# Performance work log

Hardware: AMD Instinct MI355X
Metric: run time of the kernel (lower is better)

Reference implementation:

```python
import jax, jax.numpy as jnp
import numpy as np

SCORE_THRESHOLD = 0.15
IOU_THRESHOLD = 0.5
MAX_OUTPUT = 10          # tf.image.non_max_suppression(..., 10, ...)
NUM_CLASSES = 80
NUM_ANCHORS = 5
NEG = -1e9               # score for suppressed / below-threshold boxes


def setup_inputs() -> dict:
    key = jax.random.key(0)
    k1, k2 = jax.random.split(key)
    preds = jax.random.normal(k1, (16, 52, 52, NUM_ANCHORS * (5 + NUM_CLASSES)), dtype=jnp.float32)
    # anchor priors in grid-cell units, typical YOLOv2 range
    anchors = jax.random.uniform(k2, (NUM_ANCHORS, 2), dtype=jnp.float32, minval=0.5, maxval=6.0)
    return {"preds": preds, "anchors": anchors}


def _decode(preds, anchors):
    """YOLOv2 head decode (the `_interpret_prediction` callable)."""
    B, H, W, _ = preds.shape
    A = anchors.shape[0]
    p = preds.reshape(B, H, W, A, 5 + NUM_CLASSES)
    gy, gx = jnp.meshgrid(jnp.arange(H, dtype=preds.dtype),
                          jnp.arange(W, dtype=preds.dtype), indexing="ij")
    grid = jnp.stack([gx, gy], axis=-1)[None, :, :, None, :]   # (1,H,W,1,2) in (x,y)
    dims = jnp.array([W, H], dtype=preds.dtype)
    box_xy = (jax.nn.sigmoid(p[..., :2]) + grid) / dims        # normalized centers
    box_wh = jnp.exp(p[..., 2:4]) * anchors[None, None, None, :, :] / dims
    box_confidence = jax.nn.sigmoid(p[..., 4:5])
    box_class_probs = jax.nn.softmax(p[..., 5:], axis=-1)
    return box_xy, box_wh, box_confidence, box_class_probs


def _iou(box, boxes):
    """IoU of one box (ymin,xmin,ymax,xmax) against all boxes [N,4]."""
    tl = jnp.maximum(box[:2], boxes[:, :2])
    br = jnp.minimum(box[2:], boxes[:, 2:])
    inter = jnp.prod(jnp.maximum(br - tl, 0.0), axis=-1)
    area1 = jnp.prod(jnp.maximum(box[2:] - box[:2], 0.0))
    area2 = jnp.prod(jnp.maximum(boxes[:, 2:] - boxes[:, :2], 0.0), axis=-1)
    return inter / (area1 + area2 - inter + 1e-9)


def reference(preds, anchors):
    box_xy, box_wh, box_confidence, box_class_probs = _decode(preds, anchors)
    box_mins = box_xy - box_wh / 2.0
    box_maxes = box_xy + box_wh / 2.0
    # (ymin, xmin, ymax, xmax), matching the K.concatenate in the source
    boxes = jnp.concatenate([box_mins[..., 1:2], box_mins[..., 0:1],
                             box_maxes[..., 1:2], box_maxes[..., 0:1]], axis=-1)
    box_scores = box_confidence * box_class_probs
    box_classes = jnp.argmax(box_scores, axis=-1)
    box_class_scores = jnp.max(box_scores, axis=-1)

    boxes = boxes.reshape(-1, 4)                       # [N,4]
    scores = box_class_scores.reshape(-1)              # [N]
    classes = box_classes.reshape(-1).astype(preds.dtype)

    # score-threshold mask: instead of boolean_mask (dynamic shape), kill scores
    live = jnp.where(scores >= SCORE_THRESHOLD, scores, NEG)

    # greedy NMS, fixed MAX_OUTPUT iterations (semantics of tf.image.non_max_suppression)
    def step(cur_scores, _):
        i = jnp.argmax(cur_scores)
        s = cur_scores[i]
        valid = s > NEG / 2
        box = boxes[i]
        ious = _iou(box, boxes)
        nxt = jnp.where(ious > IOU_THRESHOLD, NEG, cur_scores).at[i].set(NEG)
        row = jnp.where(valid,
                        jnp.concatenate([box, s[None], classes[i][None]]),
                        jnp.zeros((6,), dtype=preds.dtype))
        return nxt, row

    _, rows = jax.lax.scan(step, live, None, length=MAX_OUTPUT)
    return rows  # [10, 6] = (ymin, xmin, ymax, xmax, score, class); zero rows = padding
```

## Files before the change

### kernel.cpp

```cpp
#include <hip/hip_runtime.h>
#include <math.h>

#define A_N      5
#define GRID_HW  52
#define NCLS     80
#define CH       85
#define SCORE_T  0.15f
#define IOU_T    0.5f
#define NEGV     (-1e9f)
#define MAXOUT   10

#define BPB          32
#define TILE_FLOATS  (BPB * CH)
#define FULL_LOADS   10
#define TAIL_LANES   40

#define NMS_THREADS  256
#define NCAP         4096
#define NKA          (NCAP / NMS_THREADS)

__device__ __forceinline__ float fexp(float x) { return __expf(x); }

__device__ __forceinline__ void gload_lds16(const float* g, float* l) {
    __builtin_amdgcn_global_load_lds(
        (const __attribute__((address_space(1))) unsigned int*)g,
        (__attribute__((address_space(3))) unsigned int*)l, 16, 0, 0);
}

__global__ void init_counter_kernel(int* __restrict__ counter) {
    *counter = 0;
}

__global__ __launch_bounds__(64) void decode_kernel(
    const float* __restrict__ preds,
    const float* __restrict__ anchors,
    float4* __restrict__ pbox, float* __restrict__ pscore,
    float* __restrict__ pcls,
    int* __restrict__ counter, int N, int capacity)
{
    __shared__ __align__(16) float lds[TILE_FLOATS];

    const int tile = blockIdx.x;
    const int lane = (int)threadIdx.x;
    const float* gbase = preds + (size_t)tile * TILE_FLOATS;

#pragma unroll
    for (int i = 0; i < FULL_LOADS; ++i) {
        gload_lds16(gbase + (size_t)(i * 64 + lane) * 4, &lds[i * 256]);
    }
    if (lane < TAIL_LANES) {
        gload_lds16(gbase + (size_t)(FULL_LOADS * 64 + lane) * 4,
                    &lds[FULL_LOADS * 256]);
    }
    __syncthreads();

    const int b  = lane >> 1;
    const int h  = lane & 1;
    const int gi = tile * BPB + b;
    const float* bp = lds + b * CH;
    const float* cl = bp + 5 + h * 40;

    float m = cl[0];
    int   am = h * 40;
#pragma unroll
    for (int j = 1; j < 40; ++j) {
        float x = cl[j];
        if (x > m) { m = x; am = h * 40 + j; }
    }
    float s = 0.0f;
#pragma unroll
    for (int j = 0; j < 40; ++j) s += fexp(cl[j] - m);

    {
        float m2 = __shfl_xor(m, 1);
        float s2 = __shfl_xor(s, 1);
        int   am2 = __shfl_xor(am, 1);
        float M = fmaxf(m, m2);
        s = s * fexp(m - M) + s2 * fexp(m2 - M);
        if (m2 > m || (m2 == m && am2 < am)) am = am2;
        m = M;
    }

    float conf  = 1.0f / (1.0f + fexp(-bp[4]));
    float score = conf / s;

    bool live = (h == 0) && (gi < N) && (score >= SCORE_T);

    unsigned long long mask = __ballot(live);
    if (mask) {
        int nlive  = __popcll(mask);
        int leader = (int)__ffsll((long long)mask) - 1;
        int base_ = 0;
        if (lane == leader) base_ = atomicAdd(counter, nlive);
        base_ = __shfl(base_, leader);
        if (live) {
            int a = gi % A_N;
            int t = gi / A_N;
            int wx = t % GRID_HW;
            int hy = (t / GRID_HW) % GRID_HW;
            const float inv = 1.0f / (float)GRID_HW;
            float cx = (1.0f / (1.0f + fexp(-bp[0])) + (float)wx) * inv;
            float cy = (1.0f / (1.0f + fexp(-bp[1])) + (float)hy) * inv;
            float bw = fexp(bp[2]) * anchors[2 * a]     * inv;
            float bh = fexp(bp[3]) * anchors[2 * a + 1] * inv;

            int pos = base_ + __popcll(mask & ((1ull << lane) - 1));
            if (pos < capacity) {
                pbox[pos]   = make_float4(cy - 0.5f * bh, cx - 0.5f * bw,
                                          cy + 0.5f * bh, cx + 0.5f * bw);
                pscore[pos] = score;
                pcls[pos]   = (float)am;
            }
        }
    }
}

__global__ __launch_bounds__(NMS_THREADS) void nms_kernel(
    const float4* __restrict__ pbox, float* __restrict__ pscore,
    const float* __restrict__ pcls, const int* __restrict__ counter,
    int capacity, float* __restrict__ out)
{
    __shared__ float sy0[NCAP], sx0[NCAP], sy1[NCAP], sx1[NCAP], ssc[NCAP];
    __shared__ float psc[4];
    __shared__ int   pix[4];

    int M = *counter;
    if (M > capacity) M = capacity;
    const int tid  = (int)threadIdx.x;
    const int lane = tid & 63;
    const int wid  = tid >> 6;

    if (M <= NCAP) {
#pragma unroll
        for (int k = 0; k < NKA; ++k) {
            int j = tid + (k << 8);
            if (j < M) {
                float4 bx = pbox[j];
                sy0[j] = bx.x; sx0[j] = bx.y; sy1[j] = bx.z; sx1[j] = bx.w;
                ssc[j] = pscore[j];
            } else {
                ssc[j] = -INFINITY;
            }
        }
        __syncthreads();

        for (int it = 0; it < MAXOUT; ++it) {
            float bs = -INFINITY; int bi = -1;
#pragma unroll
            for (int k = 0; k < NKA; ++k) {
                int j = tid + (k << 8);
                float v = ssc[j];
                if (v > bs) { bs = v; bi = j; }
            }
#pragma unroll
            for (int off = 32; off; off >>= 1) {
                float os = __shfl_xor(bs, off);
                int   oi = __shfl_xor(bi, off);
                if (os > bs || (os == bs && oi != -1 && (bi == -1 || oi < bi))) {
                    bs = os; bi = oi;
                }
            }
            if (lane == 0) { psc[wid] = bs; pix[wid] = bi; }
            __syncthreads();

            bs = psc[0]; bi = pix[0];
#pragma unroll
            for (int w = 1; w < 4; ++w) {
                float os = psc[w]; int oi = pix[w];
                if (os > bs || (os == bs && oi != -1 && (bi == -1 || oi < bi))) {
                    bs = os; bi = oi;
                }
            }
            bool valid = (bi >= 0) && (bs > NEGV * 0.5f);

            if (tid == 0) {
                if (valid) {
                    out[it*6+0] = sy0[bi]; out[it*6+1] = sx0[bi];
                    out[it*6+2] = sy1[bi]; out[it*6+3] = sx1[bi];
                    out[it*6+4] = bs;      out[it*6+5] = pcls[bi];
                } else {
                    out[it*6+0] = 0.f; out[it*6+1] = 0.f; out[it*6+2] = 0.f;
                    out[it*6+3] = 0.f; out[it*6+4] = 0.f; out[it*6+5] = 0.f;
                }
            }

            if (valid) {
                float wy0 = sy0[bi], wx0 = sx0[bi], wy1 = sy1[bi], wx1 = sx1[bi];
                float a1 = fmaxf(wy1 - wy0, 0.f) * fmaxf(wx1 - wx0, 0.f);
#pragma unroll
                for (int k = 0; k < NKA; ++k) {
                    int j = tid + (k << 8);
                    if (j == bi) ssc[j] = NEGV;
                    float ty = fmaxf(wy0, sy0[j]);
                    float tx = fmaxf(wx0, sx0[j]);
                    float by = fminf(wy1, sy1[j]);
                    float bx = fminf(wx1, sx1[j]);
                    float inter = fmaxf(by - ty, 0.f) * fmaxf(bx - tx, 0.f);
                    float a2 = fmaxf(sy1[j] - sy0[j], 0.f) * fmaxf(sx1[j] - sx0[j], 0.f);
                    float iou = inter / (a1 + a2 - inter + 1e-9f);
                    if (iou > IOU_T && j < M) ssc[j] = NEGV;
                }
            }
            __syncthreads();
        }
    } else {
        for (int it = 0; it < MAXOUT; ++it) {
            float bs = -INFINITY; int bi = -1;
            for (int j = tid; j < M; j += NMS_THREADS) {
                float v = pscore[j];
                if (v > bs) { bs = v; bi = j; }
            }
#pragma unroll
            for (int off = 32; off; off >>= 1) {
                float os = __shfl_xor(bs, off);
                int   oi = __shfl_xor(bi, off);
                if (os > bs || (os == bs && oi != -1 && (bi == -1 || oi < bi))) {
                    bs = os; bi = oi;
                }
            }
            if (lane == 0) { psc[wid] = bs; pix[wid] = bi; }
            __syncthreads();
            bs = psc[0]; bi = pix[0];
#pragma unroll
            for (int w = 1; w < 4; ++w) {
                float os = psc[w]; int oi = pix[w];
                if (os > bs || (os == bs && oi != -1 && (bi == -1 || oi < bi))) {
                    bs = os; bi = oi;
                }
            }
            bool valid = (bi >= 0) && (bs > NEGV * 0.5f);
            if (tid == 0) {
                if (valid) {
                    float4 bx = pbox[bi];
                    out[it*6+0] = bx.x; out[it*6+1] = bx.y;
                    out[it*6+2] = bx.z; out[it*6+3] = bx.w;
                    out[it*6+4] = bs;   out[it*6+5] = pcls[bi];
                    pscore[bi] = NEGV;
                } else {
                    out[it*6+0] = 0.f; out[it*6+1] = 0.f; out[it*6+2] = 0.f;
                    out[it*6+3] = 0.f; out[it*6+4] = 0.f; out[it*6+5] = 0.f;
                }
            }
            __syncthreads();
            if (valid) {
                float4 wb = pbox[bi];
                float a1 = fmaxf(wb.z - wb.x, 0.f) * fmaxf(wb.w - wb.y, 0.f);
                for (int j = tid; j < M; j += NMS_THREADS) {
                    float4 bj = pbox[j];
                    float ty = fmaxf(wb.x, bj.x);
                    float tx = fmaxf(wb.y, bj.y);
                    float by = fminf(wb.z, bj.z);
                    float bx = fminf(wb.w, bj.w);
                    float inter = fmaxf(by - ty, 0.f) * fmaxf(bx - tx, 0.f);
                    float a2 = fmaxf(bj.z - bj.x, 0.f) * fmaxf(bj.w - bj.y, 0.f);
                    float iou = inter / (a1 + a2 - inter + 1e-9f);
                    if (iou > IOU_T) pscore[j] = NEGV;
                }
            }
            __syncthreads();
        }
    }
}

extern "C" void kernel_launch(void* const* d_in, const int* in_sizes, int n_in,
                              void* d_out, int out_size, void* d_ws, size_t ws_size,
                              hipStream_t stream) {
    (void)n_in; (void)out_size;
    const float* preds   = (const float*)d_in[0];
    const float* anchors = (const float*)d_in[1];
    float* out = (float*)d_out;

    int N = in_sizes[0] / CH;

    char* ws = (char*)d_ws;
    int* counter = (int*)ws;
    size_t avail = (ws_size > 64) ? (ws_size - 64) : 0;
    long long cap = (long long)(avail / (sizeof(float4) + 2 * sizeof(float)));
    if (cap > N) cap = N;
    if (cap < 0) cap = 0;
    int capacity = (int)cap;

    float4* pbox  = (float4*)(ws + 64);
    float* pscore = (float*)(pbox + capacity);
    float* pcls   = pscore + capacity;

    init_counter_kernel<<<1, 1, 0, stream>>>(counter);

    int nTiles = (N + BPB - 1) / BPB;
    decode_kernel<<<nTiles, 64, 0, stream>>>(
        preds, anchors, pbox, pscore, pcls, counter, N, capacity);
    nms_kernel<<<1, NMS_THREADS, 0, stream>>>(
        pbox, pscore, pcls, counter, capacity, out);
}
```

Baseline: 76.58 us.

## Enlarge decode blocks, fuse softmax pass, and widen NMS to 1024 threads

After: 67.58 us (median of 4 runs). 11.8% less time.

```diff
diff --git a/kernel.cpp b/kernel.cpp
--- a/kernel.cpp
+++ b/kernel.cpp
@@ -10,14 +10,15 @@
 #define NEGV     (-1e9f)
 #define MAXOUT   10
 
-#define BPB          32
+#define BPB          128
+#define DEC_THREADS  256
 #define TILE_FLOATS  (BPB * CH)
-#define FULL_LOADS   10
-#define TAIL_LANES   40
-
-#define NMS_THREADS  256
+#define WAVE_FLOATS  (TILE_FLOATS / 4)
+#define WAVE_FULL    10
+#define WAVE_TAIL    40
+
+#define NMS_THREADS  1024
 #define NCAP         4096
-#define NKA          (NCAP / NMS_THREADS)
 
 __device__ __forceinline__ float fexp(float x) { return __expf(x); }
 
@@ -31,7 +32,7 @@
     *counter = 0;
 }
 
-__global__ __launch_bounds__(64) void decode_kernel(
+__global__ __launch_bounds__(DEC_THREADS) void decode_kernel(
     const float* __restrict__ preds,
     const float* __restrict__ anchors,
     float4* __restrict__ pbox, float* __restrict__ pscore,
@@ -41,48 +42,48 @@
     __shared__ __align__(16) float lds[TILE_FLOATS];
 
     const int tile = blockIdx.x;
-    const int lane = (int)threadIdx.x;
-    const float* gbase = preds + (size_t)tile * TILE_FLOATS;
-
-#pragma unroll
-    for (int i = 0; i < FULL_LOADS; ++i) {
-        gload_lds16(gbase + (size_t)(i * 64 + lane) * 4, &lds[i * 256]);
-    }
-    if (lane < TAIL_LANES) {
-        gload_lds16(gbase + (size_t)(FULL_LOADS * 64 + lane) * 4,
-                    &lds[FULL_LOADS * 256]);
+    const int lane = (int)threadIdx.x & 63;
+    const int wid  = (int)threadIdx.x >> 6;
+
+    const float* gbase = preds + (size_t)tile * TILE_FLOATS + wid * WAVE_FLOATS;
+    float* lbase = lds + wid * WAVE_FLOATS;
+
+#pragma unroll
+    for (int i = 0; i < WAVE_FULL; ++i) {
+        gload_lds16(gbase + (size_t)(i * 64 + lane) * 4, lbase + i * 256);
+    }
+    if (lane < WAVE_TAIL) {
+        gload_lds16(gbase + (size_t)(WAVE_FULL * 64 + lane) * 4,
+                    lbase + WAVE_FULL * 256);
     }
     __syncthreads();
 
-    const int b  = lane >> 1;
-    const int h  = lane & 1;
+    const int b  = (int)threadIdx.x >> 1;
+    const int h  = (int)threadIdx.x & 1;
     const int gi = tile * BPB + b;
     const float* bp = lds + b * CH;
     const float* cl = bp + 5 + h * 40;
 
-    float m = cl[0];
+    float s = 0.0f;
+    float m = -INFINITY;
     int   am = h * 40;
 #pragma unroll
-    for (int j = 1; j < 40; ++j) {
+    for (int j = 0; j < 40; ++j) {
         float x = cl[j];
+        s += fexp(x);
         if (x > m) { m = x; am = h * 40 + j; }
     }
-    float s = 0.0f;
-#pragma unroll
-    for (int j = 0; j < 40; ++j) s += fexp(cl[j] - m);
 
     {
         float m2 = __shfl_xor(m, 1);
         float s2 = __shfl_xor(s, 1);
         int   am2 = __shfl_xor(am, 1);
-        float M = fmaxf(m, m2);
-        s = s * fexp(m - M) + s2 * fexp(m2 - M);
-        if (m2 > m || (m2 == m && am2 < am)) am = am2;
-        m = M;
+        s += s2;
+        if (m2 > m || (m2 == m && am2 < am)) { m = m2; am = am2; }
     }
 
     float conf  = 1.0f / (1.0f + fexp(-bp[4]));
-    float score = conf / s;
+    float score = conf * fexp(m) / s;
 
     bool live = (h == 0) && (gi < N) && (score >= SCORE_T);
 
@@ -121,8 +122,8 @@
     int capacity, float* __restrict__ out)
 {
     __shared__ float sy0[NCAP], sx0[NCAP], sy1[NCAP], sx1[NCAP], ssc[NCAP];
-    __shared__ float psc[4];
-    __shared__ int   pix[4];
+    __shared__ float psc[16];
+    __shared__ int   pix[16];
 
     int M = *counter;
     if (M > capacity) M = capacity;
@@ -131,9 +132,8 @@
     const int wid  = tid >> 6;
 
     if (M <= NCAP) {
-#pragma unroll
-        for (int k = 0; k < NKA; ++k) {
-            int j = tid + (k << 8);
+        int Mr = (M + NMS_THREADS - 1) & ~(NMS_THREADS - 1);
+        for (int j = tid; j < Mr; j += NMS_THREADS) {
             if (j < M) {
                 float4 bx = pbox[j];
                 sy0[j] = bx.x; sx0[j] = bx.y; sy1[j] = bx.z; sx1[j] = bx.w;
@@ -146,9 +146,7 @@
 
         for (int it = 0; it < MAXOUT; ++it) {
             float bs = -INFINITY; int bi = -1;
-#pragma unroll
-            for (int k = 0; k < NKA; ++k) {
-                int j = tid + (k << 8);
+            for (int j = tid; j < Mr; j += NMS_THREADS) {
                 float v = ssc[j];
                 if (v > bs) { bs = v; bi = j; }
             }
@@ -165,7 +163,7 @@
 
             bs = psc[0]; bi = pix[0];
 #pragma unroll
-            for (int w = 1; w < 4; ++w) {
+            for (int w = 1; w < 16; ++w) {
                 float os = psc[w]; int oi = pix[w];
                 if (os > bs || (os == bs && oi != -1 && (bi == -1 || oi < bi))) {
                     bs = os; bi = oi;
@@ -187,18 +185,18 @@
             if (valid) {
                 float wy0 = sy0[bi], wx0 = sx0[bi], wy1 = sy1[bi], wx1 = sx1[bi];
                 float a1 = fmaxf(wy1 - wy0, 0.f) * fmaxf(wx1 - wx0, 0.f);
-#pragma unroll
-                for (int k = 0; k < NKA; ++k) {
-                    int j = tid + (k << 8);
+                for (int j = tid; j < Mr; j += NMS_THREADS) {
                     if (j == bi) ssc[j] = NEGV;
-                    float ty = fmaxf(wy0, sy0[j]);
-                    float tx = fmaxf(wx0, sx0[j]);
-                    float by = fminf(wy1, sy1[j]);
-                    float bx = fminf(wx1, sx1[j]);
-                    float inter = fmaxf(by - ty, 0.f) * fmaxf(bx - tx, 0.f);
-                    float a2 = fmaxf(sy1[j] - sy0[j], 0.f) * fmaxf(sx1[j] - sx0[j], 0.f);
-                    float iou = inter / (a1 + a2 - inter + 1e-9f);
-                    if (iou > IOU_T && j < M) ssc[j] = NEGV;
+                    if (j < M) {
+                        float ty = fmaxf(wy0, sy0[j]);
+                        float tx = fmaxf(wx0, sx0[j]);
+                        float by = fminf(wy1, sy1[j]);
+                        float bx = fminf(wx1, sx1[j]);
+                        float inter = fmaxf(by - ty, 0.f) * fmaxf(bx - tx, 0.f);
+                        float a2 = fmaxf(sy1[j] - sy0[j], 0.f) * fmaxf(sx1[j] - sx0[j], 0.f);
+                        float iou = inter / (a1 + a2 - inter + 1e-9f);
+                        if (iou > IOU_T) ssc[j] = NEGV;
+                    }
                 }
             }
             __syncthreads();
@@ -222,7 +220,7 @@
             __syncthreads();
             bs = psc[0]; bi = pix[0];
 #pragma unroll
-            for (int w = 1; w < 4; ++w) {
+            for (int w = 1; w < 16; ++w) {
                 float os = psc[w]; int oi = pix[w];
                 if (os > bs || (os == bs && oi != -1 && (bi == -1 || oi < bi))) {
                     bs = os; bi = oi;
@@ -287,7 +285,7 @@
     init_counter_kernel<<<1, 1, 0, stream>>>(counter);
 
     int nTiles = (N + BPB - 1) / BPB;
-    decode_kernel<<<nTiles, 64, 0, stream>>>(
+    decode_kernel<<<nTiles, DEC_THREADS, 0, stream>>>(
         preds, anchors, pbox, pscore, pcls, counter, N, capacity);
     nms_kernel<<<1, NMS_THREADS, 0, stream>>>(
         pbox, pscore, pcls, counter, capacity, out);
```
